# Kernel optimization log

Hardware: AMD Instinct MI355X
Metric: run time of the kernel (lower is better)

The kernel has to match this reference:

```python
import jax, jax.numpy as jnp
import numpy as np

A, NL, LD, F, W, DEPTH = 128, 16, 256, 256, 1024, 4
CH, CHD = 8, 64   # cross-attn heads / head_dim
SH, SHD = 8, 32   # latent self-attn heads / head_dim
FF = 256          # 2**ceil(log2(latent_dim))
FLAT = NL * LD


def _ln(x, g, b, eps=1e-5):
    m = x.mean(-1, keepdims=True)
    v = ((x - m) ** 2).mean(-1, keepdims=True)
    return (x - m) * jax.lax.rsqrt(v + eps) * g + b


def _attn(q_in, kv, wq, wk, wv, wo, bo, h, hd):
    b, s, _ = q_in.shape
    t = kv.shape[1]
    q = (q_in @ wq.T).reshape(b, s, h, hd)
    k = (kv @ wk.T).reshape(b, t, h, hd)
    v = (kv @ wv.T).reshape(b, t, h, hd)
    p = jax.nn.softmax(jnp.einsum('bihd,bjhd->bhij', q, k) * (hd ** -0.5), axis=-1)
    o = jnp.einsum('bhij,bjhd->bihd', p, v).reshape(b, s, h * hd)
    return o @ wo.T + bo


def _block(q, kv, p, h, hd):
    wq, wk, wv, wo, bo, g1, b1, fw1, fb1, fw2, fb2, g2, b2 = p
    z = _ln(q + _attn(q, kv, wq, wk, wv, wo, bo, h, hd), g1, b1)
    ff = jax.nn.relu(z @ fw1.T + fb1) @ fw2.T + fb2
    return _ln(z + ff, g2, b2)


def setup_inputs() -> dict:
    key = jax.random.key(0)
    ks = iter(jax.random.split(key, 40))
    def rn(shape, s=0.02):
        return jax.random.normal(next(ks), shape, jnp.float32) * s
    return {
        'x': jax.random.normal(next(ks), (A, W, F), jnp.float32),
        'z': jax.random.normal(next(ks), (A, NL, LD), jnp.float32),
        'c_wq': rn((CH * CHD, LD)), 'c_wk': rn((CH * CHD, F)), 'c_wv': rn((CH * CHD, F)),
        'c_wo': rn((LD, CH * CHD)), 'c_bo': jnp.zeros((LD,), jnp.float32),
        'c_ln1_g': jnp.ones((LD,), jnp.float32), 'c_ln1_b': jnp.zeros((LD,), jnp.float32),
        'c_ff_w1': rn((FF, LD)), 'c_ff_b1': jnp.zeros((FF,), jnp.float32),
        'c_ff_w2': rn((LD, FF)), 'c_ff_b2': jnp.zeros((LD,), jnp.float32),
        'c_ln2_g': jnp.ones((LD,), jnp.float32), 'c_ln2_b': jnp.zeros((LD,), jnp.float32),
        's_wq': rn((DEPTH, SH * SHD, LD)), 's_wk': rn((DEPTH, SH * SHD, LD)),
        's_wv': rn((DEPTH, SH * SHD, LD)), 's_wo': rn((DEPTH, LD, SH * SHD)),
        's_bo': jnp.zeros((DEPTH, LD), jnp.float32),
        's_ln1_g': jnp.ones((DEPTH, LD), jnp.float32), 's_ln1_b': jnp.zeros((DEPTH, LD), jnp.float32),
        's_ff_w1': rn((DEPTH, FF, LD)), 's_ff_b1': jnp.zeros((DEPTH, FF), jnp.float32),
        's_ff_w2': rn((DEPTH, LD, FF)), 's_ff_b2': jnp.zeros((DEPTH, LD), jnp.float32),
        's_ln2_g': jnp.ones((DEPTH, LD), jnp.float32), 's_ln2_b': jnp.zeros((DEPTH, LD), jnp.float32),
        'q_w': rn((FLAT, FLAT)), 'q_b': jnp.zeros((FLAT,), jnp.float32),
        'k_w': rn((FLAT, FLAT)), 'k_b': jnp.zeros((FLAT,), jnp.float32),
        'v_w': rn((FLAT, FLAT)), 'v_b': jnp.zeros((FLAT,), jnp.float32),
    }


def reference(x, z, c_wq, c_wk, c_wv, c_wo, c_bo, c_ln1_g, c_ln1_b, c_ff_w1, c_ff_b1,
              c_ff_w2, c_ff_b2, c_ln2_g, c_ln2_b,
              s_wq, s_wk, s_wv, s_wo, s_bo, s_ln1_g, s_ln1_b, s_ff_w1, s_ff_b1,
              s_ff_w2, s_ff_b2, s_ln2_g, s_ln2_b,
              q_w, q_b, k_w, k_b, v_w, v_b):
    z_prior = z
    # NOTE: original LSRE.forward computes cross-attention but assigns the
    # result to x and never uses it. Replicated faithfully (dead computation;
    # output does not depend on x or the cross-attn params).
    _ = _block(z, x, (c_wq, c_wk, c_wv, c_wo, c_bo, c_ln1_g, c_ln1_b,
                      c_ff_w1, c_ff_b1, c_ff_w2, c_ff_b2, c_ln2_g, c_ln2_b), CH, CHD)
    zc = z
    sp = (s_wq, s_wk, s_wv, s_wo, s_bo, s_ln1_g, s_ln1_b,
          s_ff_w1, s_ff_b1, s_ff_w2, s_ff_b2, s_ln2_g, s_ln2_b)
    for i in range(DEPTH):
        zc = _block(zc, zc, tuple(p[i] for p in sp), SH, SHD)
    # CANN: asset-to-asset attention; broadcast-mul-then-sum == attn @ v
    zf = zc.reshape(A, FLAT)
    q = zf @ q_w.T + q_b
    k = zf @ k_w.T + k_b
    v = zf @ v_w.T + v_b
    attn = jax.nn.softmax((q @ k.T) * (LD ** -0.5), axis=-1)
    h = (attn @ v).reshape(A, NL, LD)
    return (h, z_prior)
```

## Files before the change

kernel.cpp:

```cpp
#include <hip/hip_runtime.h>
#include <math.h>

typedef __bf16 bf16x8 __attribute__((ext_vector_type(8)));
typedef __bf16 bf16x4 __attribute__((ext_vector_type(4)));
typedef float  f32x4  __attribute__((ext_vector_type(4)));

#define MFMA(a,b,c) __builtin_amdgcn_mfma_f32_16x16x32_bf16((a),(b),(c),0,0,0)

#define A_N   128
#define LDIM  256
#define FLATD 4096

__global__ __launch_bounds__(256) void k_cvt_w(
        const float* __restrict__ s0, const float* __restrict__ s1,
        const float* __restrict__ s2, const float* __restrict__ s3,
        const float* __restrict__ s4, const float* __restrict__ s5,
        __bf16* __restrict__ W) {
    const int g    = blockIdx.x * 256 + threadIdx.x;
    const int lane = g & 63;
    const int L    = g >> 6;
    const int lp   = L / 1536;
    const int rem  = L - lp * 1536;
    const int w    = rem / 96;
    const int li   = rem - w * 96;

    int m, ks, hl;
    if (li < 48)      { ks = li / 6; int sub = li - ks * 6; m = sub >> 1; hl = sub & 1; }
    else if (li < 64) { int i = li - 48; m = 3; ks = i >> 1; hl = i & 1; }
    else if (li < 80) { int i = li - 64; m = 4; ks = i >> 1; hl = i & 1; }
    else              { int i = li - 80; m = 5; ks = i >> 1; hl = i & 1; }

    const float* s;
    switch (m) {
        case 0: s = s0; break; case 1: s = s1; break; case 2: s = s2; break;
        case 3: s = s3; break; case 4: s = s4; break; default: s = s5; break;
    }
    const float* src = s + lp * 65536 + (w * 16 + (lane & 15)) * 256
                         + ks * 32 + (lane >> 4) * 8;
    float4 x = ((const float4*)src)[0], y = ((const float4*)src)[1];
    float v[8] = {x.x, x.y, x.z, x.w, y.x, y.y, y.z, y.w};
    bf16x8 o;
    #pragma unroll
    for (int j = 0; j < 8; ++j) {
        __bf16 hh = (__bf16)v[j];
        o[j] = hl ? (__bf16)(v[j] - (float)hh) : hh;
    }
    *(bf16x8*)(W + (size_t)g * 8) = o;
}

__global__ __launch_bounds__(1024) void k_latent(
    const float* __restrict__ z,
    const __bf16* __restrict__ Wswz,
    const float* __restrict__ boa,
    const float* __restrict__ g1a, const float* __restrict__ b1a,
    const float* __restrict__ fb1a, const float* __restrict__ fb2a,
    const float* __restrict__ g2a, const float* __restrict__ b2a,
    float* __restrict__ zprior, __bf16* __restrict__ Zbh, __bf16* __restrict__ Zbl)
{
    __shared__ __align__(16) char arena[57856];
    float*  zf  = (float*)arena;
    __bf16* zbh = (__bf16*)(arena + 16384);
    __bf16* zbl = (__bf16*)(arena + 24832);
    __bf16* Ph  = (__bf16*)(arena + 16384);
    __bf16* Qh  = (__bf16*)(arena + 33280);
    __bf16* ob  = Qh;
    __bf16* Kh  = (__bf16*)(arena + 41472);
    __bf16* Vt  = (__bf16*)(arena + 49664);

    const int a    = blockIdx.x;
    const int t    = threadIdx.x;
    const int w    = t >> 6;
    const int lane = t & 63;
    const int q    = lane >> 4;
    const int r    = lane & 15;
    const int nc   = w * 16;
    const int head = w >> 1;
    const int hc   = (w & 1) * 16;

    {
        int row = t >> 6, col = (t & 63) * 4;
        const float4 x = *(const float4*)(z + (size_t)a * 4096 + row * 256 + col);
        *(float4*)(zprior + (size_t)a * 4096 + row * 256 + col) = x;
        float v[4] = {x.x, x.y, x.z, x.w};
        float*  zr = zf  + row * 256 + col;
        __bf16* zh = zbh + row * 264 + col;
        __bf16* zl = zbl + row * 264 + col;
        #pragma unroll
        for (int j = 0; j < 4; ++j) {
            zr[j] = v[j];
            __bf16 hh = (__bf16)v[j];
            zh[j] = hh;
            zl[j] = (__bf16)(v[j] - (float)hh);
        }
    }
    __syncthreads();

    auto do_ln = [&](const float* g, const float* bb) {
        int col = lane * 4;
        float* zr = zf + w * 256 + col;
        float4 v4 = *(const float4*)zr;
        float v[4] = {v4.x, v4.y, v4.z, v4.w};
        float s1 = 0.f, s2 = 0.f;
        #pragma unroll
        for (int j = 0; j < 4; ++j) { s1 += v[j]; s2 += v[j]*v[j]; }
        #pragma unroll
        for (int o = 1; o <= 32; o <<= 1) {
            s1 += __shfl_xor(s1, o);
            s2 += __shfl_xor(s2, o);
        }
        float mean = s1 * (1.0f/256.0f);
        float var  = s2 * (1.0f/256.0f) - mean * mean;
        float inv  = rsqrtf(var + 1e-5f);
        float4 g4 = *(const float4*)(g + col);
        float4 b4 = *(const float4*)(bb + col);
        float gg[4] = {g4.x, g4.y, g4.z, g4.w};
        float bbv[4] = {b4.x, b4.y, b4.z, b4.w};
        __bf16* zh = zbh + w * 264 + col;
        __bf16* zl = zbl + w * 264 + col;
        float y[4];
        #pragma unroll
        for (int j = 0; j < 4; ++j) {
            y[j] = (v[j] - mean) * inv * gg[j] + bbv[j];
            __bf16 hh = (__bf16)y[j];
            zh[j] = hh;
            zl[j] = (__bf16)(y[j] - (float)hh);
        }
        *(float4*)zr = (float4){y[0], y[1], y[2], y[3]};
    };

    const f32x4 zero4 = {0.f, 0.f, 0.f, 0.f};
    bf16x8 zer8;
    #pragma unroll
    for (int j = 0; j < 8; ++j) zer8[j] = (__bf16)0.0f;

    for (int lp = 0; lp < 4; ++lp) {
        const float* bo  = boa  + lp*256;
        const float* g1  = g1a  + lp*256; const float* b1 = b1a + lp*256;
        const float* fb1 = fb1a + lp*256; const float* fb2 = fb2a + lp*256;
        const float* g2  = g2a  + lp*256; const float* b2 = b2a + lp*256;

        const __bf16* wsl = Wswz + (size_t)(lp * 16 + w) * 49152 + (size_t)lane * 8;
        #define WCHUNK(idx) (*(const bf16x8*)(wsl + (idx) * 512))

        const __bf16* zA_h = zbh + r * 264 + q * 8;
        const __bf16* zA_l = zbl + r * 264 + q * 8;
        const __bf16* oA   = ob  + r * 264 + q * 8;

        {
            f32x4 aq = zero4, ak = zero4, av = zero4;
            #pragma unroll
            for (int ks = 0; ks < 8; ++ks) {
                bf16x8 afh = *(const bf16x8*)(zA_h + ks*32);
                bf16x8 afl = *(const bf16x8*)(zA_l + ks*32);
                bf16x8 qh = WCHUNK(ks*6 + 0);
                bf16x8 ql = WCHUNK(ks*6 + 1);
                bf16x8 kh = WCHUNK(ks*6 + 2);
                bf16x8 kl = WCHUNK(ks*6 + 3);
                bf16x8 vh = WCHUNK(ks*6 + 4);
                bf16x8 vl = WCHUNK(ks*6 + 5);
                aq = MFMA(afh, qh, aq); aq = MFMA(afl, qh, aq); aq = MFMA(afh, ql, aq);
                ak = MFMA(afh, kh, ak); ak = MFMA(afl, kh, ak); ak = MFMA(afh, kl, ak);
                av = MFMA(afh, vh, av); av = MFMA(afl, vh, av); av = MFMA(afh, vl, av);
            }
            #pragma unroll
            for (int i = 0; i < 4; ++i) {
                int m = q*4 + i;
                Qh[(head*16 + m)*32 + hc + r] = (__bf16)aq[i];
                Kh[(head*16 + m)*32 + hc + r] = (__bf16)ak[i];
                Vt[(head*32 + hc + r)*16 + m] = (__bf16)av[i];
            }
        }
        __syncthreads();

        if (w < 8) {
            bf16x8 qa = *(const bf16x8*)(Qh + (w*16 + r)*32 + q*8);
            bf16x8 ka = *(const bf16x8*)(Kh + (w*16 + r)*32 + q*8);
            f32x4 s = MFMA(qa, ka, zero4);
            #pragma unroll
            for (int i = 0; i < 4; ++i) {
                float sc = s[i] * 0.17677669529663687f;
                float mx = sc;
                #pragma unroll
                for (int o = 1; o <= 8; o <<= 1) mx = fmaxf(mx, __shfl_xor(mx, o, 16));
                float e = __expf(sc - mx);
                float sm = e;
                #pragma unroll
                for (int o = 1; o <= 8; o <<= 1) sm += __shfl_xor(sm, o, 16);
                Ph[(w*16 + q*4 + i)*32 + r]      = (__bf16)(e / sm);
                Ph[(w*16 + q*4 + i)*32 + 16 + r] = (__bf16)0.0f;
            }
        }
        __syncthreads();

        {
            int ph = w & 7, vnt = w >> 3;
            bf16x8 pa = *(const bf16x8*)(Ph + (ph*16 + r)*32 + q*8);
            bf16x8 vb = (q < 2)
                ? *(const bf16x8*)(Vt + (ph*32 + vnt*16 + r)*16 + q*8) : zer8;
            f32x4 o = MFMA(pa, vb, zero4);
            #pragma unroll
            for (int i = 0; i < 4; ++i)
                ob[(q*4 + i)*264 + ph*32 + vnt*16 + r] = (__bf16)o[i];
        }
        __syncthreads();

        {
            f32x4 acc = zero4;
            #pragma unroll
            for (int ks = 0; ks < 8; ++ks) {
                bf16x8 af = *(const bf16x8*)(oA + ks*32);
                bf16x8 bh = WCHUNK(48 + ks*2);
                bf16x8 bl = WCHUNK(49 + ks*2);
                acc = MFMA(af, bh, acc);
                acc = MFMA(af, bl, acc);
            }
            #pragma unroll
            for (int i = 0; i < 4; ++i) {
                int row = q*4 + i, col = nc + r;
                zf[row*256 + col] = acc[i] + bo[col] + zf[row*256 + col];
            }
        }
        __syncthreads();
        do_ln(g1, b1);
        __syncthreads();

        {
            f32x4 acc = zero4;
            #pragma unroll
            for (int ks = 0; ks < 8; ++ks) {
                bf16x8 afh = *(const bf16x8*)(zA_h + ks*32);
                bf16x8 afl = *(const bf16x8*)(zA_l + ks*32);
                bf16x8 bh  = WCHUNK(64 + ks*2);
                bf16x8 bl  = WCHUNK(65 + ks*2);
                acc = MFMA(afh, bh, acc);
                acc = MFMA(afl, bh, acc);
                acc = MFMA(afh, bl, acc);
            }
            #pragma unroll
            for (int i = 0; i < 4; ++i) {
                int row = q*4 + i, col = nc + r;
                ob[row*264 + col] = (__bf16)fmaxf(acc[i] + fb1[col], 0.0f);
            }
        }
        __syncthreads();

        {
            f32x4 acc = zero4;
            #pragma unroll
            for (int ks = 0; ks < 8; ++ks) {
                bf16x8 af = *(const bf16x8*)(oA + ks*32);
                bf16x8 bh = WCHUNK(80 + ks*2);
                bf16x8 bl = WCHUNK(81 + ks*2);
                acc = MFMA(af, bh, acc);
                acc = MFMA(af, bl, acc);
            }
            #pragma unroll
            for (int i = 0; i < 4; ++i) {
                int row = q*4 + i, col = nc + r;
                zf[row*256 + col] = acc[i] + fb2[col] + zf[row*256 + col];
            }
        }
        __syncthreads();
        do_ln(g2, b2);
        __syncthreads();
        #undef WCHUNK
    }

    {
        int row = t >> 6, col = (t & 63) * 4;
        *(bf16x4*)(Zbh + (size_t)a * 4096 + row * 256 + col) =
            *(const bf16x4*)(zbh + row * 264 + col);
        *(bf16x4*)(Zbl + (size_t)a * 4096 + row * 256 + col) =
            *(const bf16x4*)(zbl + row * 264 + col);
    }
}

__global__ __launch_bounds__(256) void k_cann_gemm(
    const __bf16* __restrict__ Zh, const __bf16* __restrict__ Zl,
    const float* __restrict__ W0, const float* __restrict__ W1, const float* __restrict__ W2,
    const float* __restrict__ b0, const float* __restrict__ b1, const float* __restrict__ b2,
    float* __restrict__ C0, float* __restrict__ C1, float* __restrict__ C2)
{
    const float* W; const float* bias; float* C;
    if (blockIdx.y == 0)      { W = W0; bias = b0; C = C0; }
    else if (blockIdx.y == 1) { W = W1; bias = b1; C = C1; }
    else                      { W = W2; bias = b2; C = C2; }

    __shared__ __bf16 Ash[128 * 72];
    __shared__ __bf16 Asl[128 * 72];
    __shared__ __bf16 Bsh[32 * 72];
    __shared__ __bf16 Bsl[32 * 72];

    const int t = threadIdx.x;
    const int w = t >> 6, lane = t & 63, q = lane >> 4, r = lane & 15;
    const int n0 = blockIdx.x * 32;
    const int m0 = w * 32;
    const int br = t >> 3, bc = t & 7;

    const f32x4 zero4 = {0.f, 0.f, 0.f, 0.f};
    f32x4 acc[2][2] = {{zero4, zero4}, {zero4, zero4}};

    for (int k0 = 0; k0 < FLATD; k0 += 64) {
        #pragma unroll
        for (int l = 0; l < 4; ++l) {
            int idx = t + l * 256;
            int rr = idx >> 3, cc = idx & 7;
            *(bf16x8*)(Ash + rr*72 + cc*8) =
                *(const bf16x8*)(Zh + (size_t)rr * FLATD + k0 + cc*8);
            *(bf16x8*)(Asl + rr*72 + cc*8) =
                *(const bf16x8*)(Zl + (size_t)rr * FLATD + k0 + cc*8);
        }
        {
            const float4* wp = (const float4*)(W + (size_t)(n0 + br) * FLATD + k0 + bc*8);
            float4 x = wp[0], y = wp[1];
            float v[8] = {x.x, x.y, x.z, x.w, y.x, y.y, y.z, y.w};
            bf16x8 h, l;
            #pragma unroll
            for (int j = 0; j < 8; ++j) {
                __bf16 hh = (__bf16)v[j];
                h[j] = hh;
                l[j] = (__bf16)(v[j] - (float)hh);
            }
            *(bf16x8*)(Bsh + br*72 + bc*8) = h;
            *(bf16x8*)(Bsl + br*72 + bc*8) = l;
        }
        __syncthreads();
        #pragma unroll
        for (int ks = 0; ks < 2; ++ks) {
            bf16x8 a0h = *(const bf16x8*)(Ash + (m0 + r)*72      + ks*32 + q*8);
            bf16x8 a1h = *(const bf16x8*)(Ash + (m0 + 16 + r)*72 + ks*32 + q*8);
            bf16x8 a0l = *(const bf16x8*)(Asl + (m0 + r)*72      + ks*32 + q*8);
            bf16x8 a1l = *(const bf16x8*)(Asl + (m0 + 16 + r)*72 + ks*32 + q*8);
            bf16x8 g0h = *(const bf16x8*)(Bsh + r*72             + ks*32 + q*8);
            bf16x8 g1h = *(const bf16x8*)(Bsh + (16 + r)*72      + ks*32 + q*8);
            bf16x8 g0l = *(const bf16x8*)(Bsl + r*72             + ks*32 + q*8);
            bf16x8 g1l = *(const bf16x8*)(Bsl + (16 + r)*72      + ks*32 + q*8);
            acc[0][0] = MFMA(a0h, g0h, acc[0][0]);
            acc[0][0] = MFMA(a0l, g0h, acc[0][0]);
            acc[0][0] = MFMA(a0h, g0l, acc[0][0]);
            acc[0][1] = MFMA(a0h, g1h, acc[0][1]);
            acc[0][1] = MFMA(a0l, g1h, acc[0][1]);
            acc[0][1] = MFMA(a0h, g1l, acc[0][1]);
            acc[1][0] = MFMA(a1h, g0h, acc[1][0]);
            acc[1][0] = MFMA(a1l, g0h, acc[1][0]);
            acc[1][0] = MFMA(a1h, g0l, acc[1][0]);
            acc[1][1] = MFMA(a1h, g1h, acc[1][1]);
            acc[1][1] = MFMA(a1l, g1h, acc[1][1]);
            acc[1][1] = MFMA(a1h, g1l, acc[1][1]);
        }
        __syncthreads();
    }

    if (blockIdx.y == 1) {
        #pragma unroll
        for (int mi = 0; mi < 2; ++mi)
            #pragma unroll
            for (int ni = 0; ni < 2; ++ni)
                #pragma unroll
                for (int i = 0; i < 4; ++i) {
                    int row = m0 + mi*16 + q*4 + i;
                    int col = n0 + ni*16 + r;
                    C[(size_t)col * 128 + row] = acc[mi][ni][i] + bias[col];
                }
    } else {
        #pragma unroll
        for (int mi = 0; mi < 2; ++mi)
            #pragma unroll
            for (int ni = 0; ni < 2; ++ni)
                #pragma unroll
                for (int i = 0; i < 4; ++i) {
                    int row = m0 + mi*16 + q*4 + i;
                    int col = n0 + ni*16 + r;
                    C[(size_t)row * FLATD + col] = acc[mi][ni][i] + bias[col];
                }
    }
}

__global__ __launch_bounds__(512) void k_cann_scores(const float* __restrict__ Q,
                              const float* __restrict__ KT,
                              float* __restrict__ P) {
    const int i0 = blockIdx.x * 2;
    const int t  = threadIdx.x;
    __shared__ float qs[2][FLATD];
    __shared__ float part[4][2][128];
    __shared__ float wred[2][2];
    __shared__ float wsum[2][2];
    {
        const float4* src = (const float4*)(Q + (size_t)i0 * FLATD);
        float4* dst = (float4*)qs;
        #pragma unroll
        for (int u = 0; u < 4; ++u) dst[t + u * 512] = src[t + u * 512];
    }
    __syncthreads();

    const int j = t & 127, ksub = t >> 7;
    const float* kp = KT + (size_t)(ksub * 1024) * 128 + j;
    const float* q0 = qs[0] + ksub * 1024;
    const float* q1 = qs[1] + ksub * 1024;
    float a0 = 0.0f, a1 = 0.0f;
    #pragma unroll 8
    for (int k = 0; k < 1024; ++k) {
        float kv = kp[(size_t)k * 128];
        a0 += q0[k] * kv;
        a1 += q1[k] * kv;
    }
    part[ksub][0][j] = a0;
    part[ksub][1][j] = a1;
    __syncthreads();

    float v = 0.0f, e = 0.0f;
    const int i = t >> 7;
    if (t < 256)
        v = (part[0][i][j] + part[1][i][j] + part[2][i][j] + part[3][i][j]) * 0.0625f;

    float mx = (t < 256) ? v : -3.4e38f;
    #pragma unroll
    for (int o = 32; o; o >>= 1) mx = fmaxf(mx, __shfl_xor(mx, o));
    if (t < 256 && (j & 63) == 0) wred[i][j >> 6] = mx;
    __syncthreads();
    if (t < 256) {
        mx = fmaxf(wred[i][0], wred[i][1]);
        e = __expf(v - mx);
    }
    float sum = e;
    #pragma unroll
    for (int o = 32; o; o >>= 1) sum += __shfl_xor(sum, o);
    if (t < 256 && (j & 63) == 0) wsum[i][j >> 6] = sum;
    __syncthreads();
    if (t < 256) {
        sum = wsum[i][0] + wsum[i][1];
        P[(size_t)(i0 + i) * 128 + j] = e / sum;
    }
}

__global__ __launch_bounds__(256) void k_cann_out(const float* __restrict__ P,
                           const float* __restrict__ V,
                           float* __restrict__ H) {
    const int i0 = blockIdx.y * 8;
    const int t  = threadIdx.x;
    const int nb = blockIdx.x * 1024 + t * 4;
    __shared__ float ps[128][8];
    #pragma unroll
    for (int u = 0; u < 4; ++u) {
        int e = t + u * 256;
        int i = e >> 7, j = e & 127;
        ps[j][i] = P[(size_t)(i0 + i) * 128 + j];
    }
    __syncthreads();

    f32x4 acc[8];
    #pragma unroll
    for (int i = 0; i < 8; ++i) acc[i] = (f32x4){0.f, 0.f, 0.f, 0.f};

    for (int j = 0; j < 128; ++j) {
        float4 vv = *(const float4*)(V + (size_t)j * FLATD + nb);
        f32x4 v4 = {vv.x, vv.y, vv.z, vv.w};
        float4 pa = *(const float4*)&ps[j][0];
        float4 pb = *(const float4*)&ps[j][4];
        acc[0] += pa.x * v4; acc[1] += pa.y * v4;
        acc[2] += pa.z * v4; acc[3] += pa.w * v4;
        acc[4] += pb.x * v4; acc[5] += pb.y * v4;
        acc[6] += pb.z * v4; acc[7] += pb.w * v4;
    }
    #pragma unroll
    for (int i = 0; i < 8; ++i) {
        f32x4 a = acc[i];
        *(float4*)(H + (size_t)(i0 + i) * FLATD + nb) =
            (float4){a[0], a[1], a[2], a[3]};
    }
}

extern "C" void kernel_launch(void* const* d_in, const int* in_sizes, int n_in,
                              void* d_out, int out_size, void* d_ws, size_t ws_size,
                              hipStream_t stream) {
    (void)in_sizes; (void)n_in; (void)out_size; (void)ws_size;

    const float* z      = (const float*)d_in[1];
    const float* s_wq   = (const float*)d_in[15];
    const float* s_wk   = (const float*)d_in[16];
    const float* s_wv   = (const float*)d_in[17];
    const float* s_wo   = (const float*)d_in[18];
    const float* s_bo   = (const float*)d_in[19];
    const float* s_ln1g = (const float*)d_in[20];
    const float* s_ln1b = (const float*)d_in[21];
    const float* s_fw1  = (const float*)d_in[22];
    const float* s_fb1  = (const float*)d_in[23];
    const float* s_fw2  = (const float*)d_in[24];
    const float* s_fb2  = (const float*)d_in[25];
    const float* s_ln2g = (const float*)d_in[26];
    const float* s_ln2b = (const float*)d_in[27];
    const float* q_w    = (const float*)d_in[28];
    const float* q_b    = (const float*)d_in[29];
    const float* k_w    = (const float*)d_in[30];
    const float* k_b    = (const float*)d_in[31];
    const float* v_w    = (const float*)d_in[32];
    const float* v_b    = (const float*)d_in[33];

    float* out    = (float*)d_out;
    float* Hout   = out;
    float* Zprior = out + 524288;

    char* w8 = (char*)d_ws;
    __bf16* Wswz = (__bf16*)w8;
    float*  Qb  = (float*)w8;
    float*  Kb  = (float*)(w8 + 2097152);
    float*  Vb  = (float*)(w8 + 4194304);
    __bf16* Zbh = (__bf16*)(w8 + 6291456);
    __bf16* Zbl = (__bf16*)(w8 + 7340032);
    float*  Pm  = (float*)(w8 + 8388608);

    k_cvt_w<<<1536, 256, 0, stream>>>(s_wq, s_wk, s_wv, s_wo, s_fw1, s_fw2, Wswz);

    k_latent<<<A_N, 1024, 0, stream>>>(z, Wswz, s_bo, s_ln1g, s_ln1b,
                                       s_fb1, s_fb2, s_ln2g, s_ln2b,
                                       Zprior, Zbh, Zbl);

    k_cann_gemm<<<dim3(FLATD / 32, 3), 256, 0, stream>>>(Zbh, Zbl, q_w, k_w, v_w,
                                                         q_b, k_b, v_b, Qb, Kb, Vb);

    k_cann_scores<<<A_N / 2, 512, 0, stream>>>(Qb, Kb, Pm);
    k_cann_out<<<dim3(4, 16), 256, 0, stream>>>(Pm, Vb, Hout);
}
```

Baseline: 522.0 us.

## Double-buffer CANN projection GEMM and widen N tile to 64 with 512 threads

Restructures the CANN QKV projection GEMM to prefetch the next K-chunk of Z and W into registers while MFMAs run on the current LDS buffer, using two LDS buffers and one barrier per step. The block tile grows to 64 output columns with 8 waves, which halves the number of blocks and the redundant reloads of the shared Z tile. Both changes aim to hide global load latency and cut per-block A traffic. The cost is more LDS, more register pressure and fewer blocks (192) spread across the CUs.

Measured after the change: 519.9 us. No clear change (-0.4%).

```diff
diff --git a/kernel.cpp b/kernel.cpp
--- a/kernel.cpp
+++ b/kernel.cpp
@@ -275,7 +275,7 @@
     }
 }
 
-__global__ __launch_bounds__(256) void k_cann_gemm(
+__global__ __launch_bounds__(512) void k_cann_gemm(
     const __bf16* __restrict__ Zh, const __bf16* __restrict__ Zl,
     const float* __restrict__ W0, const float* __restrict__ W1, const float* __restrict__ W2,
     const float* __restrict__ b0, const float* __restrict__ b1, const float* __restrict__ b2,
@@ -286,55 +286,62 @@
     else if (blockIdx.y == 1) { W = W1; bias = b1; C = C1; }
     else                      { W = W2; bias = b2; C = C2; }
 
-    __shared__ __bf16 Ash[128 * 72];
-    __shared__ __bf16 Asl[128 * 72];
-    __shared__ __bf16 Bsh[32 * 72];
-    __shared__ __bf16 Bsl[32 * 72];
+    __shared__ __bf16 AshB[2][128 * 72];
+    __shared__ __bf16 AslB[2][128 * 72];
+    __shared__ __bf16 BshB[2][64 * 72];
+    __shared__ __bf16 BslB[2][64 * 72];
 
     const int t = threadIdx.x;
     const int w = t >> 6, lane = t & 63, q = lane >> 4, r = lane & 15;
-    const int n0 = blockIdx.x * 32;
-    const int m0 = w * 32;
-    const int br = t >> 3, bc = t & 7;
+    const int n0 = blockIdx.x * 64;
+    const int m0 = (w >> 1) * 32;
+    const int nw = (w & 1) * 32;
+
+    const int ar0 = t >> 3, ac = (t & 7) * 8;
+    const int br  = t >> 3, bc = (t & 7) * 8;
+
+    struct Stage { bf16x8 a0h, a1h, a0l, a1l; float4 wx, wy; };
+
+    auto issue = [&](Stage& S, int k0) {
+        S.a0h = *(const bf16x8*)(Zh + (size_t)ar0        * FLATD + k0 + ac);
+        S.a1h = *(const bf16x8*)(Zh + (size_t)(ar0 + 64) * FLATD + k0 + ac);
+        S.a0l = *(const bf16x8*)(Zl + (size_t)ar0        * FLATD + k0 + ac);
+        S.a1l = *(const bf16x8*)(Zl + (size_t)(ar0 + 64) * FLATD + k0 + ac);
+        const float4* wp = (const float4*)(W + (size_t)(n0 + br) * FLATD + k0 + bc);
+        S.wx = wp[0]; S.wy = wp[1];
+    };
+
+    auto wr = [&](const Stage& S, int b) {
+        *(bf16x8*)(&AshB[b][ar0 * 72 + ac])        = S.a0h;
+        *(bf16x8*)(&AshB[b][(ar0 + 64) * 72 + ac]) = S.a1h;
+        *(bf16x8*)(&AslB[b][ar0 * 72 + ac])        = S.a0l;
+        *(bf16x8*)(&AslB[b][(ar0 + 64) * 72 + ac]) = S.a1l;
+        float v[8] = {S.wx.x, S.wx.y, S.wx.z, S.wx.w, S.wy.x, S.wy.y, S.wy.z, S.wy.w};
+        bf16x8 h, l;
+        #pragma unroll
+        for (int j = 0; j < 8; ++j) {
+            __bf16 hh = (__bf16)v[j];
+            h[j] = hh;
+            l[j] = (__bf16)(v[j] - (float)hh);
+        }
+        *(bf16x8*)(&BshB[b][br * 72 + bc]) = h;
+        *(bf16x8*)(&BslB[b][br * 72 + bc]) = l;
+    };
 
     const f32x4 zero4 = {0.f, 0.f, 0.f, 0.f};
     f32x4 acc[2][2] = {{zero4, zero4}, {zero4, zero4}};
 
-    for (int k0 = 0; k0 < FLATD; k0 += 64) {
-        #pragma unroll
-        for (int l = 0; l < 4; ++l) {
-            int idx = t + l * 256;
-            int rr = idx >> 3, cc = idx & 7;
-            *(bf16x8*)(Ash + rr*72 + cc*8) =
-                *(const bf16x8*)(Zh + (size_t)rr * FLATD + k0 + cc*8);
-            *(bf16x8*)(Asl + rr*72 + cc*8) =
-                *(const bf16x8*)(Zl + (size_t)rr * FLATD + k0 + cc*8);
-        }
-        {
-            const float4* wp = (const float4*)(W + (size_t)(n0 + br) * FLATD + k0 + bc*8);
-            float4 x = wp[0], y = wp[1];
-            float v[8] = {x.x, x.y, x.z, x.w, y.x, y.y, y.z, y.w};
-            bf16x8 h, l;
-            #pragma unroll
-            for (int j = 0; j < 8; ++j) {
-                __bf16 hh = (__bf16)v[j];
-                h[j] = hh;
-                l[j] = (__bf16)(v[j] - (float)hh);
-            }
-            *(bf16x8*)(Bsh + br*72 + bc*8) = h;
-            *(bf16x8*)(Bsl + br*72 + bc*8) = l;
-        }
-        __syncthreads();
+    auto mfma_phase = [&](int b) {
         #pragma unroll
         for (int ks = 0; ks < 2; ++ks) {
-            bf16x8 a0h = *(const bf16x8*)(Ash + (m0 + r)*72      + ks*32 + q*8);
-            bf16x8 a1h = *(const bf16x8*)(Ash + (m0 + 16 + r)*72 + ks*32 + q*8);
-            bf16x8 a0l = *(const bf16x8*)(Asl + (m0 + r)*72      + ks*32 + q*8);
-            bf16x8 a1l = *(const bf16x8*)(Asl + (m0 + 16 + r)*72 + ks*32 + q*8);
-            bf16x8 g0h = *(const bf16x8*)(Bsh + r*72             + ks*32 + q*8);
-            bf16x8 g1h = *(const bf16x8*)(Bsh + (16 + r)*72      + ks*32 + q*8);
-            bf16x8 g0l = *(const bf16x8*)(Bsl + r*72             + ks*32 + q*8);
-            bf16x8 g1l = *(const bf16x8*)(Bsl + (16 + r)*72      + ks*32 + q*8);
+            bf16x8 a0h = *(const bf16x8*)(&AshB[b][(m0 + r)      * 72 + ks*32 + q*8]);
+            bf16x8 a1h = *(const bf16x8*)(&AshB[b][(m0 + 16 + r) * 72 + ks*32 + q*8]);
+            bf16x8 a0l = *(const bf16x8*)(&AslB[b][(m0 + r)      * 72 + ks*32 + q*8]);
+            bf16x8 a1l = *(const bf16x8*)(&AslB[b][(m0 + 16 + r) * 72 + ks*32 + q*8]);
+            bf16x8 g0h = *(const bf16x8*)(&BshB[b][(nw + r)      * 72 + ks*32 + q*8]);
+            bf16x8 g1h = *(const bf16x8*)(&BshB[b][(nw + 16 + r) * 72 + ks*32 + q*8]);
+            bf16x8 g0l = *(const bf16x8*)(&BslB[b][(nw + r)      * 72 + ks*32 + q*8]);
+            bf16x8 g1l = *(const bf16x8*)(&BslB[b][(nw + 16 + r) * 72 + ks*32 + q*8]);
             acc[0][0] = MFMA(a0h, g0h, acc[0][0]);
             acc[0][0] = MFMA(a0l, g0h, acc[0][0]);
             acc[0][0] = MFMA(a0h, g0l, acc[0][0]);
@@ -348,8 +355,41 @@
             acc[1][1] = MFMA(a1l, g1h, acc[1][1]);
             acc[1][1] = MFMA(a1h, g1l, acc[1][1]);
         }
-        __syncthreads();
-    }
+    };
+
+    #define LGKM0_BAR() do {                                      \
+        asm volatile("s_waitcnt lgkmcnt(0)" ::: "memory");        \
+        __builtin_amdgcn_sched_barrier(0);                        \
+        __builtin_amdgcn_s_barrier();                             \
+        __builtin_amdgcn_sched_barrier(0);                        \
+    } while (0)
+
+    Stage S0, S1;
+    issue(S0, 0);
+    issue(S1, 64);
+    wr(S0, 0);
+    LGKM0_BAR();
+
+    int cur = 0;
+    int kk  = 128;
+    for (int it = 0; it < 31; ++it) {
+        issue(S0, kk); kk += 64;
+        mfma_phase(cur);
+        wr(S1, cur ^ 1);
+        LGKM0_BAR();
+        cur ^= 1;
+        issue(S1, kk); kk += 64;
+        mfma_phase(cur);
+        wr(S0, cur ^ 1);
+        LGKM0_BAR();
+        cur ^= 1;
+    }
+    mfma_phase(cur);
+    wr(S1, cur ^ 1);
+    LGKM0_BAR();
+    cur ^= 1;
+    mfma_phase(cur);
+    #undef LGKM0_BAR
 
     if (blockIdx.y == 1) {
         #pragma unroll
@@ -359,7 +399,7 @@
                 #pragma unroll
                 for (int i = 0; i < 4; ++i) {
                     int row = m0 + mi*16 + q*4 + i;
-                    int col = n0 + ni*16 + r;
+                    int col = n0 + nw + ni*16 + r;
                     C[(size_t)col * 128 + row] = acc[mi][ni][i] + bias[col];
                 }
     } else {
@@ -370,7 +410,7 @@
                 #pragma unroll
                 for (int i = 0; i < 4; ++i) {
                     int row = m0 + mi*16 + q*4 + i;
-                    int col = n0 + ni*16 + r;
+                    int col = n0 + nw + ni*16 + r;
                     C[(size_t)row * FLATD + col] = acc[mi][ni][i] + bias[col];
                 }
     }
@@ -515,7 +555,7 @@
                                        s_fb1, s_fb2, s_ln2g, s_ln2b,
                                        Zprior, Zbh, Zbl);
 
-    k_cann_gemm<<<dim3(FLATD / 32, 3), 256, 0, stream>>>(Zbh, Zbl, q_w, k_w, v_w,
+    k_cann_gemm<<<dim3(FLATD / 64, 3), 512, 0, stream>>>(Zbh, Zbl, q_w, k_w, v_w,
                                                          q_b, k_b, v_b, Qb, Kb, Vb);
 
     k_cann_scores<<<A_N / 2, 512, 0, stream>>>(Qb, Kb, Pm);
```
